# Optimization experiments

Measured on AMD Instinct MI355X. Metric: run time of the kernel, lower is better.

## Reference

```python
import jax, jax.numpy as jnp
import numpy as np

S, H, F_, E = 4096, 1024, 4096, 8
CAP_FACTOR = 1.25  # router_capacity_factor_train (module defaults to training mode)
MIN_CAP = 4


def _capacity(s, e):
    c = int(2 * CAP_FACTOR * s / e)  # floor(k * cap_factor * S / E), k=2
    c += c % 2
    return max(c, MIN_CAP)


def setup_inputs() -> dict:
    key = jax.random.key(0)
    k0, k1, k2, k3, k4 = jax.random.split(key, 5)
    return {
        "hidden_states": jax.random.normal(k0, (S, H), jnp.float32),
        "gate_w": jax.random.normal(k1, (H, E), jnp.float32) * 0.02,
        "w_gate": jax.random.normal(k2, (E, H, 2 * F_), jnp.float32) * 0.02,
        "w_up": jax.random.normal(k3, (E, H, F_), jnp.float32) * 0.02,
        "w_down": jax.random.normal(k4, (E, F_, H), jnp.float32) * 0.02,
    }


def reference(hidden_states, gate_w, w_gate, w_up, w_down):
    tokens = hidden_states.reshape(-1, hidden_states.shape[-1]).astype(jnp.float32)  # [S,H]
    s, h = tokens.shape
    e = gate_w.shape[1]
    cap = _capacity(s, e)

    # --- router (top-2 with capacity) ---
    logits = tokens @ gate_w                       # [S,E] fp32
    probs = jax.nn.softmax(logits, axis=-1)
    top1 = jnp.argmax(probs, axis=-1)              # [S]
    mask1 = jax.nn.one_hot(top1, e, dtype=jnp.int32)
    top2 = jnp.argmax(jnp.where(mask1 > 0, -jnp.inf, probs), axis=-1)
    mask2 = jax.nn.one_hot(top2, e, dtype=jnp.int32)

    rank1 = jnp.cumsum(mask1, axis=0) - 1          # position within expert queue
    rank2 = jnp.cumsum(mask2, axis=0) - 1 + jnp.sum(mask1, axis=0, keepdims=True)
    mask1 = mask1 * (rank1 < cap)
    mask2 = mask2 * (rank2 < cap)
    r1 = jnp.sum(mask1 * rank1, axis=-1)           # [S] slot index (0 if dropped)
    r2 = jnp.sum(mask2 * rank2, axis=-1)

    w1 = jnp.take_along_axis(mask1 * probs, top1[:, None], 1)[:, 0]  # 0 if dropped
    w2 = jnp.take_along_axis(mask2 * probs, top2[:, None], 1)[:, 0]
    m1 = jnp.take_along_axis(mask1, top1[:, None], 1)[:, 0].astype(jnp.float32)
    m2 = jnp.take_along_axis(mask2, top2[:, None], 1)[:, 0].astype(jnp.float32)

    idx = jnp.arange(s)
    cb_weight = (jnp.zeros((s, e, cap), jnp.float32)
                 .at[idx, top1, r1].add(w1)
                 .at[idx, top2, r2].add(w2))       # [S,E,C]
    sec_mask = (jnp.zeros((s, e, cap), jnp.float32)
                .at[idx, top1, r1].add(m1)
                .at[idx, top2, r2].add(m2))        # [S,E,C] (0/1)

    # --- dispatch (dense matmul against one-hot capacity mask, as in source) ---
    dispatch = jnp.einsum('sec,sh->ech', sec_mask, tokens)  # [E,C,H]

    # --- per-expert SwiGLU MLP (grouped over experts) ---
    g = jnp.einsum('ech,ehf->ecf', dispatch, w_gate)        # [E,C,2F]
    x1, x2 = jnp.split(g, 2, axis=-1)
    u = jnp.einsum('ech,ehf->ecf', dispatch, w_up)          # [E,C,F]
    act = x1 * (x2 * jax.nn.sigmoid(x2)) * u
    expert_out = jnp.einsum('ecf,efh->ech', act, w_down)    # [E,C,H]

    # --- combine ---
    out = jnp.einsum('sec,ech->sh', cb_weight, expert_out)  # [S,H]
    return out.reshape(hidden_states.shape)
```

## Files before the change

kernel.cpp:

```cpp
#include <hip/hip_runtime.h>
#include <hip/hip_fp16.h>

#define S_TOK 4096
#define HDIM  1024
#define FDIM  4096
#define NEXP  8
#define CAPV  1280

typedef _Float16 half8  __attribute__((ext_vector_type(8)));
typedef _Float16 half4v __attribute__((ext_vector_type(4)));
typedef _Float16 half2v __attribute__((ext_vector_type(2)));
typedef float    floatx4 __attribute__((ext_vector_type(4)));

__device__ __forceinline__ void gld_lds16(const _Float16* g, _Float16* l) {
  __builtin_amdgcn_global_load_lds(
      (const __attribute__((address_space(1))) unsigned int*)g,
      (__attribute__((address_space(3))) unsigned int*)l, 16, 0, 0);
}

__global__ __launch_bounds__(256) void transpose_convert(
    const float* __restrict__ W, _Float16* __restrict__ Wt, int Kd, int Nd)
{
  __shared__ float tile[64][65];
  const size_t ebase = (size_t)blockIdx.z * Kd * Nd;
  const float* Wp = W + ebase;
  _Float16* Wtp = Wt + ebase;
  const int n0 = blockIdx.x * 64, k0 = blockIdx.y * 64;
  const int tid = threadIdx.x;
#pragma unroll
  for (int r = 0; r < 16; ++r) {
    int idx = r * 256 + tid;
    int kk = idx >> 6, nn = idx & 63;
    tile[kk][nn] = Wp[(size_t)(k0 + kk) * Nd + (n0 + nn)];
  }
  __syncthreads();
#pragma unroll
  for (int r = 0; r < 8; ++r) {
    int idx = (r * 256 + tid) * 2;
    int kk = idx & 63, nn = idx >> 6;
    half2v hv;
    hv[0] = (_Float16)tile[kk][nn];
    hv[1] = (_Float16)tile[kk + 1][nn];
    *(half2v*)(Wtp + (size_t)(n0 + nn) * Kd + (k0 + kk)) = hv;
  }
}

__global__ __launch_bounds__(256) void router_kernel(
    const float* __restrict__ tokens, const float* __restrict__ gw,
    int* __restrict__ top1, int* __restrict__ top2,
    float* __restrict__ w1, float* __restrict__ w2)
{
  const int wave = threadIdx.x >> 6, lane = threadIdx.x & 63;
  const int s = blockIdx.x * 4 + wave;
  const float* trow = tokens + (size_t)s * HDIM;
  float acc[8] = {0.f,0.f,0.f,0.f,0.f,0.f,0.f,0.f};
  for (int h = lane; h < HDIM; h += 64) {
    float t = trow[h];
    const float4* g = (const float4*)(gw + h * 8);
    float4 g0 = g[0], g1 = g[1];
    acc[0] += t * g0.x; acc[1] += t * g0.y; acc[2] += t * g0.z; acc[3] += t * g0.w;
    acc[4] += t * g1.x; acc[5] += t * g1.y; acc[6] += t * g1.z; acc[7] += t * g1.w;
  }
#pragma unroll
  for (int e = 0; e < 8; ++e) {
    acc[e] += __shfl_down(acc[e], 32);
    acc[e] += __shfl_down(acc[e], 16);
    acc[e] += __shfl_down(acc[e], 8);
    acc[e] += __shfl_down(acc[e], 4);
    acc[e] += __shfl_down(acc[e], 2);
    acc[e] += __shfl_down(acc[e], 1);
  }
  if (lane == 0) {
    float m = acc[0];
#pragma unroll
    for (int e = 1; e < 8; ++e) m = fmaxf(m, acc[e]);
    float sum = 0.f;
#pragma unroll
    for (int e = 0; e < 8; ++e) sum += expf(acc[e] - m);
    int t1 = 0; float b1 = acc[0];
#pragma unroll
    for (int e = 1; e < 8; ++e) if (acc[e] > b1) { b1 = acc[e]; t1 = e; }
    int t2 = -1; float b2 = -1e30f;
#pragma unroll
    for (int e = 0; e < 8; ++e) if (e != t1 && acc[e] > b2) { b2 = acc[e]; t2 = e; }
    top1[s] = t1; top2[s] = t2;
    w1[s] = expf(b1 - m) / sum;
    w2[s] = expf(b2 - m) / sum;
  }
}

__global__ __launch_bounds__(256) void scan_kernel(
    const int* __restrict__ top1, const int* __restrict__ top2,
    float* __restrict__ w1, float* __restrict__ w2,
    int* __restrict__ r1, int* __restrict__ r2, int* __restrict__ src)
{
  __shared__ int lds[256][16];
  const int tid = threadIdx.x;
  for (int i = tid; i < NEXP * CAPV; i += 256) src[i] = -1;
  int c1[8] = {0,0,0,0,0,0,0,0}, c2[8] = {0,0,0,0,0,0,0,0};
  const int base = tid * 16;
  for (int j = 0; j < 16; ++j) {
    int e1 = top1[base + j], e2 = top2[base + j];
#pragma unroll
    for (int e = 0; e < 8; ++e) { c1[e] += (e1 == e); c2[e] += (e2 == e); }
  }
#pragma unroll
  for (int e = 0; e < 8; ++e) { lds[tid][e] = c1[e]; lds[tid][8 + e] = c2[e]; }
  __syncthreads();
  for (int off = 1; off < 256; off <<= 1) {
    int vals[16];
#pragma unroll
    for (int i = 0; i < 16; ++i) vals[i] = (tid >= off) ? lds[tid - off][i] : 0;
    __syncthreads();
#pragma unroll
    for (int i = 0; i < 16; ++i) lds[tid][i] += vals[i];
    __syncthreads();
  }
  int b1[8], b2[8], tot1[8];
#pragma unroll
  for (int e = 0; e < 8; ++e) {
    b1[e] = lds[tid][e] - c1[e];
    b2[e] = lds[tid][8 + e] - c2[e];
    tot1[e] = lds[255][e];
  }
  for (int j = 0; j < 16; ++j) {
    int s = base + j;
    int e1 = top1[s];
    int r = b1[e1]++;
    bool k1 = (r < CAPV);
    r1[s] = k1 ? r : 0;
    if (!k1) w1[s] = 0.f; else src[e1 * CAPV + r] = s;
    int e2 = top2[s];
    int rr = (b2[e2]++) + tot1[e2];
    bool k2 = (rr < CAPV);
    r2[s] = k2 ? rr : 0;
    if (!k2) w2[s] = 0.f; else src[e2 * CAPV + rr] = s;
  }
}

__global__ __launch_bounds__(128) void gather_kernel(
    const float* __restrict__ tokens, const int* __restrict__ src,
    _Float16* __restrict__ disp)
{
  const int slot = blockIdx.x;
  const int s = src[slot];
  _Float16* drow = disp + (size_t)slot * HDIM;
  const int t = threadIdx.x;
  if (s < 0) {
    uint4 z = make_uint4(0u, 0u, 0u, 0u);
    ((uint4*)drow)[t] = z;
  } else {
    const float4* trow = (const float4*)(tokens + (size_t)s * HDIM);
    float4 a = trow[2 * t], b = trow[2 * t + 1];
    half8 h;
    h[0] = (_Float16)a.x; h[1] = (_Float16)a.y; h[2] = (_Float16)a.z; h[3] = (_Float16)a.w;
    h[4] = (_Float16)b.x; h[5] = (_Float16)b.y; h[6] = (_Float16)b.z; h[7] = (_Float16)b.w;
    *(half8*)(drow + t * 8) = h;
  }
}

__global__ __launch_bounds__(256) void gemm_f16(
    const _Float16* __restrict__ A, const _Float16* __restrict__ B,
    _Float16* __restrict__ C, int N, int K,
    long long sA, long long sB, long long sC)
{
  __shared__ _Float16 As[128 * 64];
  __shared__ _Float16 Bs[128 * 64];
  A += (size_t)blockIdx.z * sA;
  B += (size_t)blockIdx.z * sB;
  C += (size_t)blockIdx.z * sC;
  const int bm = blockIdx.y * 128, bn = blockIdx.x * 128;
  const int tid = threadIdx.x, wave = tid >> 6, lane = tid & 63;
  const int wm = (wave & 1) << 6, wn = (wave >> 1) << 6;

  const _Float16* gA[4]; const _Float16* gB[4];
  _Float16 *lA[4], *lB[4];
#pragma unroll
  for (int j = 0; j < 4; ++j) {
    int row = ((wave << 2) + j) * 8 + (lane >> 3);
    int c = (lane & 7) ^ (row & 7);
    gA[j] = A + (size_t)(bm + row) * K + c * 8;
    gB[j] = B + (size_t)(bn + row) * K + c * 8;
    lA[j] = As + ((wave << 2) + j) * 512;
    lB[j] = Bs + ((wave << 2) + j) * 512;
  }

  floatx4 acc[4][4] = {};

  const int kTiles = K >> 6;
  for (int kt = 0; kt < kTiles; ++kt) {
#pragma unroll
    for (int j = 0; j < 4; ++j) {
      gld_lds16(gA[j], lA[j]);
      gld_lds16(gB[j], lB[j]);
      gA[j] += 64; gB[j] += 64;
    }
    __syncthreads();
#pragma unroll
    for (int ks = 0; ks < 2; ++ks) {
      half8 af[4], bf[4];
#pragma unroll
      for (int mt = 0; mt < 4; ++mt) {
        int row = wm + mt * 16 + (lane & 15);
        int cc = (ks << 2) + (lane >> 4);
        int p = cc ^ (row & 7);
        af[mt] = *(const half8*)(As + row * 64 + p * 8);
      }
#pragma unroll
      for (int nt = 0; nt < 4; ++nt) {
        int row = wn + nt * 16 + (lane & 15);
        int cc = (ks << 2) + (lane >> 4);
        int p = cc ^ (row & 7);
        bf[nt] = *(const half8*)(Bs + row * 64 + p * 8);
      }
#pragma unroll
      for (int mt = 0; mt < 4; ++mt)
#pragma unroll
        for (int nt = 0; nt < 4; ++nt)
          acc[mt][nt] = __builtin_amdgcn_mfma_f32_16x16x32_f16(af[mt], bf[nt], acc[mt][nt], 0, 0, 0);
    }
    __syncthreads();
  }

  const int q = lane >> 4, cl = lane & 15;
#pragma unroll
  for (int mt = 0; mt < 4; ++mt)
#pragma unroll
    for (int r = 0; r < 4; ++r) {
      int grow = bm + wm + mt * 16 + q * 4 + r;
      size_t rowoff = (size_t)grow * N + bn + wn + cl;
#pragma unroll
      for (int nt = 0; nt < 4; ++nt)
        C[rowoff + nt * 16] = (_Float16)acc[mt][nt][r];
    }
}

__global__ __launch_bounds__(256) void act_kernel(
    const _Float16* __restrict__ G, _Float16* __restrict__ U)
{
  const size_t idx = ((size_t)blockIdx.x * 256 + threadIdx.x) * 8;
  const size_t ec = idx >> 12;
  const int f = (int)(idx & (FDIM - 1));
  half8 x1 = *(const half8*)(G + ec * (2 * FDIM) + f);
  half8 x2 = *(const half8*)(G + ec * (2 * FDIM) + FDIM + f);
  half8 u  = *(half8*)(U + idx);
  half8 out;
#pragma unroll
  for (int i = 0; i < 8; ++i) {
    float a = (float)x1[i], b = (float)x2[i], c = (float)u[i];
    float silu = b / (1.f + expf(-b));
    out[i] = (_Float16)(a * silu * c);
  }
  *(half8*)(U + idx) = out;
}

__global__ __launch_bounds__(256) void combine_kernel(
    const _Float16* __restrict__ eo,
    const int* __restrict__ top1, const int* __restrict__ top2,
    const float* __restrict__ w1, const float* __restrict__ w2,
    const int* __restrict__ r1, const int* __restrict__ r2,
    float* __restrict__ out)
{
  const int s = blockIdx.x;
  const int e1 = top1[s], e2 = top2[s];
  const float a = w1[s], b = w2[s];
  const int q1 = r1[s], q2 = r2[s];
  const _Float16* row1 = eo + ((size_t)e1 * CAPV + q1) * HDIM;
  const _Float16* row2 = eo + ((size_t)e2 * CAPV + q2) * HDIM;
  const int t = threadIdx.x;
  half4v h1 = *(const half4v*)(row1 + t * 4);
  half4v h2 = *(const half4v*)(row2 + t * 4);
  float4 v;
  v.x = a * (float)h1[0] + b * (float)h2[0];
  v.y = a * (float)h1[1] + b * (float)h2[1];
  v.z = a * (float)h1[2] + b * (float)h2[2];
  v.w = a * (float)h1[3] + b * (float)h2[3];
  *(float4*)(out + (size_t)s * HDIM + t * 4) = v;
}

extern "C" void kernel_launch(void* const* d_in, const int* in_sizes, int n_in,
                              void* d_out, int out_size, void* d_ws, size_t ws_size,
                              hipStream_t stream) {
  const float* hs     = (const float*)d_in[0];
  const float* gate_w = (const float*)d_in[1];
  const float* w_gate = (const float*)d_in[2];
  const float* w_up   = (const float*)d_in[3];
  const float* w_down = (const float*)d_in[4];
  float* out = (float*)d_out;

  char* ws = (char*)d_ws;
  size_t off = 0;
  _Float16* WT_GATE = (_Float16*)(ws + off); off += (size_t)NEXP * 2 * FDIM * HDIM * 2;
  _Float16* WT_UP   = (_Float16*)(ws + off); off += (size_t)NEXP * FDIM * HDIM * 2;
  _Float16* WT_DOWN = (_Float16*)(ws + off); off += (size_t)NEXP * HDIM * FDIM * 2;
  _Float16* DISP    = (_Float16*)(ws + off); off += (size_t)NEXP * CAPV * HDIM * 2;
  _Float16* G       = (_Float16*)(ws + off); off += (size_t)NEXP * CAPV * 2 * FDIM * 2;
  _Float16* U       = (_Float16*)(ws + off); off += (size_t)NEXP * CAPV * FDIM * 2;
  _Float16* EO      = (_Float16*)(ws + off); off += (size_t)NEXP * CAPV * HDIM * 2;
  int*   TOP1 = (int*)(ws + off);   off += S_TOK * 4;
  int*   TOP2 = (int*)(ws + off);   off += S_TOK * 4;
  int*   R1   = (int*)(ws + off);   off += S_TOK * 4;
  int*   R2   = (int*)(ws + off);   off += S_TOK * 4;
  float* W1   = (float*)(ws + off); off += S_TOK * 4;
  float* W2   = (float*)(ws + off); off += S_TOK * 4;
  int*   SRC  = (int*)(ws + off);   off += NEXP * CAPV * 4;

  transpose_convert<<<dim3(2 * FDIM / 64, HDIM / 64, NEXP), 256, 0, stream>>>(w_gate, WT_GATE, HDIM, 2 * FDIM);
  transpose_convert<<<dim3(FDIM / 64, HDIM / 64, NEXP), 256, 0, stream>>>(w_up, WT_UP, HDIM, FDIM);
  transpose_convert<<<dim3(HDIM / 64, FDIM / 64, NEXP), 256, 0, stream>>>(w_down, WT_DOWN, FDIM, HDIM);

  router_kernel<<<S_TOK / 4, 256, 0, stream>>>(hs, gate_w, TOP1, TOP2, W1, W2);
  scan_kernel<<<1, 256, 0, stream>>>(TOP1, TOP2, W1, W2, R1, R2, SRC);
  gather_kernel<<<NEXP * CAPV, 128, 0, stream>>>(hs, SRC, DISP);

  gemm_f16<<<dim3(2 * FDIM / 128, CAPV / 128, NEXP), 256, 0, stream>>>(
      DISP, WT_GATE, G, 2 * FDIM, HDIM,
      (long long)CAPV * HDIM, (long long)2 * FDIM * HDIM, (long long)CAPV * 2 * FDIM);
  gemm_f16<<<dim3(FDIM / 128, CAPV / 128, NEXP), 256, 0, stream>>>(
      DISP, WT_UP, U, FDIM, HDIM,
      (long long)CAPV * HDIM, (long long)FDIM * HDIM, (long long)CAPV * FDIM);
  act_kernel<<<(NEXP * CAPV * FDIM) / (256 * 8), 256, 0, stream>>>(G, U);
  gemm_f16<<<dim3(HDIM / 128, CAPV / 128, NEXP), 256, 0, stream>>>(
      U, WT_DOWN, EO, HDIM, FDIM,
      (long long)CAPV * FDIM, (long long)HDIM * FDIM, (long long)CAPV * HDIM);

  combine_kernel<<<S_TOK, 256, 0, stream>>>(EO, TOP1, TOP2, W1, W2, R1, R2, out);
}
```

Measured before the change: 1.071 ms.

## Fuse gate/up GEMMs with SwiGLU epilogue and vectorize weight transpose

Replaces the separate gate GEMM, up GEMM and elementwise activation kernel with one kernel. For each 64-column F tile it computes the x1, x2 and up products from a shared A tile and applies SwiGLU in registers before writing, so the G and U intermediates never round-trip through memory. The weight transpose-convert now uses float4 loads and half8 stores, and the gather processes two slots per block. The fused kernel keeps three accumulator sets and loads three B tiles per K step, which raises register and LDS pressure and may lower occupancy.

```diff
diff --git a/kernel.cpp b/kernel.cpp
--- a/kernel.cpp
+++ b/kernel.cpp
@@ -9,7 +9,6 @@
 
 typedef _Float16 half8  __attribute__((ext_vector_type(8)));
 typedef _Float16 half4v __attribute__((ext_vector_type(4)));
-typedef _Float16 half2v __attribute__((ext_vector_type(2)));
 typedef float    floatx4 __attribute__((ext_vector_type(4)));
 
 __device__ __forceinline__ void gld_lds16(const _Float16* g, _Float16* l) {
@@ -28,20 +27,24 @@
   const int n0 = blockIdx.x * 64, k0 = blockIdx.y * 64;
   const int tid = threadIdx.x;
 #pragma unroll
-  for (int r = 0; r < 16; ++r) {
-    int idx = r * 256 + tid;
-    int kk = idx >> 6, nn = idx & 63;
-    tile[kk][nn] = Wp[(size_t)(k0 + kk) * Nd + (n0 + nn)];
+  for (int r = 0; r < 4; ++r) {
+    int l = r * 256 + tid;
+    int n4 = l & 15, kk = l >> 4;
+    float4 v = *(const float4*)(Wp + (size_t)(k0 + kk) * Nd + n0 + n4 * 4);
+    tile[kk][n4 * 4 + 0] = v.x;
+    tile[kk][n4 * 4 + 1] = v.y;
+    tile[kk][n4 * 4 + 2] = v.z;
+    tile[kk][n4 * 4 + 3] = v.w;
   }
   __syncthreads();
 #pragma unroll
-  for (int r = 0; r < 8; ++r) {
-    int idx = (r * 256 + tid) * 2;
-    int kk = idx & 63, nn = idx >> 6;
-    half2v hv;
-    hv[0] = (_Float16)tile[kk][nn];
-    hv[1] = (_Float16)tile[kk + 1][nn];
-    *(half2v*)(Wtp + (size_t)(n0 + nn) * Kd + (k0 + kk)) = hv;
+  for (int r = 0; r < 2; ++r) {
+    int l = r * 256 + tid;
+    int kk8 = l & 7, nn = l >> 3;
+    half8 h;
+#pragma unroll
+    for (int j = 0; j < 8; ++j) h[j] = (_Float16)tile[kk8 * 8 + j][nn];
+    *(half8*)(Wtp + (size_t)(n0 + nn) * Kd + k0 + kk8 * 8) = h;
   }
 }
 
@@ -138,14 +141,14 @@
   }
 }
 
-__global__ __launch_bounds__(128) void gather_kernel(
+__global__ __launch_bounds__(256) void gather_kernel(
     const float* __restrict__ tokens, const int* __restrict__ src,
     _Float16* __restrict__ disp)
 {
-  const int slot = blockIdx.x;
+  const int slot = blockIdx.x * 2 + (threadIdx.x >> 7);
   const int s = src[slot];
   _Float16* drow = disp + (size_t)slot * HDIM;
-  const int t = threadIdx.x;
+  const int t = threadIdx.x & 127;
   if (s < 0) {
     uint4 z = make_uint4(0u, 0u, 0u, 0u);
     ((uint4*)drow)[t] = z;
@@ -159,6 +162,100 @@
   }
 }
 
+__global__ __launch_bounds__(256) void gemm_gateup_act(
+    const _Float16* __restrict__ A, const _Float16* __restrict__ WG,
+    const _Float16* __restrict__ WU, _Float16* __restrict__ ACT)
+{
+  __shared__ _Float16 As[128 * 64];
+  __shared__ _Float16 Bs[3][64 * 64];
+  const int e = blockIdx.z;
+  A += (size_t)e * CAPV * HDIM;
+  ACT += (size_t)e * CAPV * FDIM;
+  const _Float16* B0 = WG + (size_t)e * 2 * FDIM * HDIM;
+  const _Float16* B1 = B0 + (size_t)FDIM * HDIM;
+  const _Float16* B2 = WU + (size_t)e * FDIM * HDIM;
+  const int bm = blockIdx.y * 128, f0 = blockIdx.x * 64;
+  const int tid = threadIdx.x, wave = tid >> 6, lane = tid & 63;
+  const int wm = (wave & 1) << 6, wn = (wave >> 1) << 5;
+
+  const int subrow = lane >> 3;
+  const int cch = (lane & 7) ^ subrow;
+
+  const _Float16* gA[4]; _Float16* lA[4];
+#pragma unroll
+  for (int j = 0; j < 4; ++j) {
+    int row = j * 32 + wave * 8 + subrow;
+    gA[j] = A + (size_t)(bm + row) * HDIM + cch * 8;
+    lA[j] = As + (j * 32 + wave * 8) * 64;
+  }
+  const _Float16* gB[3][2]; _Float16* lB[3][2];
+#pragma unroll
+  for (int j = 0; j < 2; ++j) {
+    int row = j * 32 + wave * 8 + subrow;
+    gB[0][j] = B0 + (size_t)(f0 + row) * HDIM + cch * 8;
+    gB[1][j] = B1 + (size_t)(f0 + row) * HDIM + cch * 8;
+    gB[2][j] = B2 + (size_t)(f0 + row) * HDIM + cch * 8;
+#pragma unroll
+    for (int o = 0; o < 3; ++o) lB[o][j] = Bs[o] + (j * 32 + wave * 8) * 64;
+  }
+
+  floatx4 acc[3][4][2] = {};
+
+  for (int kt = 0; kt < HDIM / 64; ++kt) {
+#pragma unroll
+    for (int j = 0; j < 4; ++j) { gld_lds16(gA[j], lA[j]); gA[j] += 64; }
+#pragma unroll
+    for (int j = 0; j < 2; ++j)
+#pragma unroll
+      for (int o = 0; o < 3; ++o) { gld_lds16(gB[o][j], lB[o][j]); gB[o][j] += 64; }
+    __syncthreads();
+#pragma unroll
+    for (int ks = 0; ks < 2; ++ks) {
+      const int cc = (ks << 2) + (lane >> 4);
+      half8 af[4], bf[3][2];
+#pragma unroll
+      for (int mt = 0; mt < 4; ++mt) {
+        int row = wm + mt * 16 + (lane & 15);
+        int p = cc ^ (row & 7);
+        af[mt] = *(const half8*)(As + row * 64 + p * 8);
+      }
+#pragma unroll
+      for (int nt = 0; nt < 2; ++nt) {
+        int row = wn + nt * 16 + (lane & 15);
+        int p = cc ^ (row & 7);
+#pragma unroll
+        for (int o = 0; o < 3; ++o)
+          bf[o][nt] = *(const half8*)(Bs[o] + row * 64 + p * 8);
+      }
+#pragma unroll
+      for (int o = 0; o < 3; ++o)
+#pragma unroll
+        for (int mt = 0; mt < 4; ++mt)
+#pragma unroll
+          for (int nt = 0; nt < 2; ++nt)
+            acc[o][mt][nt] = __builtin_amdgcn_mfma_f32_16x16x32_f16(af[mt], bf[o][nt], acc[o][mt][nt], 0, 0, 0);
+    }
+    __syncthreads();
+  }
+
+  const int q = lane >> 4, cl = lane & 15;
+#pragma unroll
+  for (int mt = 0; mt < 4; ++mt)
+#pragma unroll
+    for (int r = 0; r < 4; ++r) {
+      int grow = bm + wm + mt * 16 + q * 4 + r;
+      size_t rowoff = (size_t)grow * FDIM + f0 + wn + cl;
+#pragma unroll
+      for (int nt = 0; nt < 2; ++nt) {
+        float x1 = acc[0][mt][nt][r];
+        float x2 = acc[1][mt][nt][r];
+        float u  = acc[2][mt][nt][r];
+        float sw = x2 / (1.f + __expf(-x2));
+        ACT[rowoff + nt * 16] = (_Float16)(x1 * sw * u);
+      }
+    }
+}
+
 __global__ __launch_bounds__(256) void gemm_f16(
     const _Float16* __restrict__ A, const _Float16* __restrict__ B,
     _Float16* __restrict__ C, int N, int K,
@@ -202,15 +299,13 @@
 #pragma unroll
       for (int mt = 0; mt < 4; ++mt) {
         int row = wm + mt * 16 + (lane & 15);
-        int cc = (ks << 2) + (lane >> 4);
-        int p = cc ^ (row & 7);
+        int p = ((ks << 2) + (lane >> 4)) ^ (row & 7);
         af[mt] = *(const half8*)(As + row * 64 + p * 8);
       }
 #pragma unroll
       for (int nt = 0; nt < 4; ++nt) {
         int row = wn + nt * 16 + (lane & 15);
-        int cc = (ks << 2) + (lane >> 4);
-        int p = cc ^ (row & 7);
+        int p = ((ks << 2) + (lane >> 4)) ^ (row & 7);
         bf[nt] = *(const half8*)(Bs + row * 64 + p * 8);
       }
 #pragma unroll
@@ -233,25 +328,6 @@
       for (int nt = 0; nt < 4; ++nt)
         C[rowoff + nt * 16] = (_Float16)acc[mt][nt][r];
     }
-}
-
-__global__ __launch_bounds__(256) void act_kernel(
-    const _Float16* __restrict__ G, _Float16* __restrict__ U)
-{
-  const size_t idx = ((size_t)blockIdx.x * 256 + threadIdx.x) * 8;
-  const size_t ec = idx >> 12;
-  const int f = (int)(idx & (FDIM - 1));
-  half8 x1 = *(const half8*)(G + ec * (2 * FDIM) + f);
-  half8 x2 = *(const half8*)(G + ec * (2 * FDIM) + FDIM + f);
-  half8 u  = *(half8*)(U + idx);
-  half8 out;
-#pragma unroll
-  for (int i = 0; i < 8; ++i) {
-    float a = (float)x1[i], b = (float)x2[i], c = (float)u[i];
-    float silu = b / (1.f + expf(-b));
-    out[i] = (_Float16)(a * silu * c);
-  }
-  *(half8*)(U + idx) = out;
 }
 
 __global__ __launch_bounds__(256) void combine_kernel(
@@ -294,8 +370,7 @@
   _Float16* WT_UP   = (_Float16*)(ws + off); off += (size_t)NEXP * FDIM * HDIM * 2;
   _Float16* WT_DOWN = (_Float16*)(ws + off); off += (size_t)NEXP * HDIM * FDIM * 2;
   _Float16* DISP    = (_Float16*)(ws + off); off += (size_t)NEXP * CAPV * HDIM * 2;
-  _Float16* G       = (_Float16*)(ws + off); off += (size_t)NEXP * CAPV * 2 * FDIM * 2;
-  _Float16* U       = (_Float16*)(ws + off); off += (size_t)NEXP * CAPV * FDIM * 2;
+  _Float16* ACT     = (_Float16*)(ws + off); off += (size_t)NEXP * CAPV * FDIM * 2;
   _Float16* EO      = (_Float16*)(ws + off); off += (size_t)NEXP * CAPV * HDIM * 2;
   int*   TOP1 = (int*)(ws + off);   off += S_TOK * 4;
   int*   TOP2 = (int*)(ws + off);   off += S_TOK * 4;
@@ -311,17 +386,12 @@
 
   router_kernel<<<S_TOK / 4, 256, 0, stream>>>(hs, gate_w, TOP1, TOP2, W1, W2);
   scan_kernel<<<1, 256, 0, stream>>>(TOP1, TOP2, W1, W2, R1, R2, SRC);
-  gather_kernel<<<NEXP * CAPV, 128, 0, stream>>>(hs, SRC, DISP);
-
-  gemm_f16<<<dim3(2 * FDIM / 128, CAPV / 128, NEXP), 256, 0, stream>>>(
-      DISP, WT_GATE, G, 2 * FDIM, HDIM,
-      (long long)CAPV * HDIM, (long long)2 * FDIM * HDIM, (long long)CAPV * 2 * FDIM);
-  gemm_f16<<<dim3(FDIM / 128, CAPV / 128, NEXP), 256, 0, stream>>>(
-      DISP, WT_UP, U, FDIM, HDIM,
-      (long long)CAPV * HDIM, (long long)FDIM * HDIM, (long long)CAPV * FDIM);
-  act_kernel<<<(NEXP * CAPV * FDIM) / (256 * 8), 256, 0, stream>>>(G, U);
+  gather_kernel<<<NEXP * CAPV / 2, 256, 0, stream>>>(hs, SRC, DISP);
+
+  gemm_gateup_act<<<dim3(FDIM / 64, CAPV / 128, NEXP), 256, 0, stream>>>(
+      DISP, WT_GATE, WT_UP, ACT);
   gemm_f16<<<dim3(HDIM / 128, CAPV / 128, NEXP), 256, 0, stream>>>(
-      U, WT_DOWN, EO, HDIM, FDIM,
+      ACT, WT_DOWN, EO, HDIM, FDIM,
       (long long)CAPV * FDIM, (long long)HDIM * FDIM, (long long)CAPV * HDIM);
 
   combine_kernel<<<S_TOK, 256, 0, stream>>>(EO, TOP1, TOP2, W1, W2, R1, R2, out);
```

Result: faster. 1.015 ms (-5.3%).
